# Kernel tuning notes

Measured on AMD Instinct MI355X. Metric: run time of the kernel, lower is better.

The kernel has to match this reference:

```python
import jax, jax.numpy as jnp
import numpy as np

B, LQ, LKV = 2, 2048, 2048
DQ, DKV, HID, NH = 1024, 1024, 1024, 16
HD = HID // NH
EPS = 1e-5


def setup_inputs() -> dict:
    key = jax.random.key(0)
    ks = jax.random.split(key, 12)
    s_q = 1.0 / np.sqrt(DQ)
    s_kv = 1.0 / np.sqrt(DKV)
    s_h = 1.0 / np.sqrt(HID)
    return {
        "query": jax.random.normal(ks[0], (B, LQ, DQ), jnp.float32),
        "key_value": jax.random.normal(ks[1], (B, LKV, DKV), jnp.float32),
        "Wq": jax.random.uniform(ks[2], (DQ, HID), jnp.float32, -s_q, s_q),
        "bq": jax.random.uniform(ks[3], (HID,), jnp.float32, -s_q, s_q),
        "Wk": jax.random.uniform(ks[4], (DKV, HID), jnp.float32, -s_kv, s_kv),
        "bk": jax.random.uniform(ks[5], (HID,), jnp.float32, -s_kv, s_kv),
        "Wv": jax.random.uniform(ks[6], (DKV, HID), jnp.float32, -s_kv, s_kv),
        "bv": jax.random.uniform(ks[7], (HID,), jnp.float32, -s_kv, s_kv),
        "Wo": jax.random.uniform(ks[8], (HID, DQ), jnp.float32, -s_h, s_h),
        "bo": jax.random.uniform(ks[9], (DQ,), jnp.float32, -s_h, s_h),
        "ln_gamma": jnp.ones((DQ,), jnp.float32),
        "ln_beta": jnp.zeros((DQ,), jnp.float32),
    }


def reference(query, key_value, Wq, bq, Wk, bk, Wv, bv, Wo, bo, ln_gamma, ln_beta):
    b, lq, _ = query.shape
    lkv = key_value.shape[1]
    # projections -> [b, heads, len, head_dim]
    Q = (query @ Wq + bq).reshape(b, lq, NH, HD).transpose(0, 2, 1, 3)
    K = (key_value @ Wk + bk).reshape(b, lkv, NH, HD).transpose(0, 2, 1, 3)
    V = (key_value @ Wv + bv).reshape(b, lkv, NH, HD).transpose(0, 2, 1, 3)
    scores = jnp.einsum("bhqd,bhkd->bhqk", Q, K) / jnp.sqrt(jnp.float32(HD))
    attn = jax.nn.softmax(scores, axis=-1)
    ctx = jnp.einsum("bhqk,bhkd->bhqd", attn, V)
    ctx = ctx.transpose(0, 2, 1, 3).reshape(b, lq, HID)
    out = ctx @ Wo + bo
    x = query + out
    mu = jnp.mean(x, axis=-1, keepdims=True)
    var = jnp.mean(jnp.square(x - mu), axis=-1, keepdims=True)
    return (x - mu) / jnp.sqrt(var + EPS) * ln_gamma + ln_beta
```

## Files before the change

kernel.cpp:

```cpp
#include <hip/hip_runtime.h>

typedef unsigned short u16;
typedef __bf16 bf16x8 __attribute__((ext_vector_type(8)));
typedef float f32x4 __attribute__((ext_vector_type(4)));
typedef unsigned short u16x4 __attribute__((ext_vector_type(4)));

#define LOG2E 1.44269504088896340736f
#define LDK 1040
#define LDV 2080
#define EXPM16 12599160.0f

__device__ __forceinline__ u16 f2bf(float f) {
  unsigned u = __float_as_uint(f);
  u += 0x7FFFu + ((u >> 16) & 1u);
  return (u16)(u >> 16);
}

__device__ __forceinline__ void load_lds16(const void* g, void* l) {
  __builtin_amdgcn_global_load_lds(
      (__attribute__((address_space(1))) void*)g,
      (__attribute__((address_space(3))) void*)l, 16, 0, 0);
}

__device__ __forceinline__ f32x4 mfma16(bf16x8 a, bf16x8 b, f32x4 c) {
  return __builtin_amdgcn_mfma_f32_16x16x32_bf16(a, b, c, 0, 0, 0);
}

__global__ __launch_bounds__(256) void pre_kernel(
    const float* __restrict__ q, const float* __restrict__ kv,
    u16* __restrict__ Xq, u16* __restrict__ Xkv,
    const float* __restrict__ Wq, const float* __restrict__ Wk,
    const float* __restrict__ Wv, const float* __restrict__ Wo,
    u16* __restrict__ Wqt, u16* __restrict__ Wkt,
    u16* __restrict__ Wvt, u16* __restrict__ Wot) {
  __shared__ float tile[32][33];
  const int bid = blockIdx.x;
  if (bid < 8192) {
    const int n4each = 4096 * 256;
    int i = bid * 256 + threadIdx.x;
    const float* src; u16* dst; int j;
    if (i < n4each) { src = q; dst = Xq; j = i; }
    else            { src = kv; dst = Xkv; j = i - n4each; }
    const float4 v = ((const float4*)src)[j];
    u16x4 o;
    o.x = f2bf(v.x); o.y = f2bf(v.y); o.z = f2bf(v.z); o.w = f2bf(v.w);
    ((u16x4*)dst)[j] = o;
    return;
  }
  const int t = bid - 8192;
  const int z = t >> 10, rem = t & 1023;
  const float* W; u16* Wt;
  switch (z) {
    case 0: W = Wq; Wt = Wqt; break;
    case 1: W = Wk; Wt = Wkt; break;
    case 2: W = Wv; Wt = Wvt; break;
    default: W = Wo; Wt = Wot; break;
  }
  const int tx = threadIdx.x & 31, ty = threadIdx.x >> 5;
  const int n0 = (rem & 31) * 32, k0 = (rem >> 5) * 32;
#pragma unroll
  for (int i = 0; i < 4; i++)
    tile[ty + i * 8][tx] = W[(size_t)(k0 + ty + i * 8) * 1024 + n0 + tx];
  __syncthreads();
#pragma unroll
  for (int i = 0; i < 4; i++)
    Wt[(size_t)(n0 + ty + i * 8) * 1024 + k0 + tx] = f2bf(tile[tx][ty + i * 8]);
}

__device__ __forceinline__ void gemm_tile(
    const u16* __restrict__ A, int lda, const u16* __restrict__ Bt, int ldb,
    const float* __restrict__ bias, bool brow, float scale,
    u16* __restrict__ Cb, float* __restrict__ Cf,
    int ldc, int bm, int bn, int K) {
  __shared__ alignas(16) u16 As[128 * 32];
  __shared__ alignas(16) u16 Bs[128 * 32];
  const int tid = threadIdx.x;
  const int wave = tid >> 6, lane = tid & 63;
  const int lm = lane & 15, kq = lane >> 4;
  const int g1 = tid, g2 = tid + 256;
  const u16* Ag1 = A + (size_t)(bm + (g1 >> 2)) * lda + (g1 & 3) * 8;
  const u16* Ag2 = A + (size_t)(bm + (g2 >> 2)) * lda + (g2 & 3) * 8;
  const u16* Bg1 = Bt + (size_t)(bn + (g1 >> 2)) * ldb + (g1 & 3) * 8;
  const u16* Bg2 = Bt + (size_t)(bn + (g2 >> 2)) * ldb + (g2 & 3) * 8;
  u16* lA1 = &As[g1 * 8]; u16* lA2 = &As[g2 * 8];
  u16* lB1 = &Bs[g1 * 8]; u16* lB2 = &Bs[g2 * 8];
  const int wm = (wave >> 1) * 64, wn = (wave & 1) * 64;

  f32x4 acc[4][4] = {};
  for (int k0 = 0; k0 < K; k0 += 32) {
    __syncthreads();
    load_lds16(Ag1 + k0, lA1);
    load_lds16(Ag2 + k0, lA2);
    load_lds16(Bg1 + k0, lB1);
    load_lds16(Bg2 + k0, lB2);
    __syncthreads();
    bf16x8 a[4], b[4];
#pragma unroll
    for (int t = 0; t < 4; t++)
      a[t] = *(const bf16x8*)&As[(wm + t * 16 + lm) * 32 + kq * 8];
#pragma unroll
    for (int t = 0; t < 4; t++)
      b[t] = *(const bf16x8*)&Bs[(wn + t * 16 + lm) * 32 + kq * 8];
#pragma unroll
    for (int mt = 0; mt < 4; mt++)
#pragma unroll
      for (int nt = 0; nt < 4; nt++)
        acc[mt][nt] = mfma16(a[mt], b[nt], acc[mt][nt]);
  }
#pragma unroll
  for (int mt = 0; mt < 4; mt++) {
    float rb[4];
#pragma unroll
    for (int r = 0; r < 4; r++)
      rb[r] = (bias && brow) ? bias[bm + wm + mt * 16 + kq * 4 + r] : 0.f;
#pragma unroll
    for (int nt = 0; nt < 4; nt++) {
      const int col = bn + wn + nt * 16 + lm;
      const float cb = (bias && !brow) ? bias[col] : 0.f;
#pragma unroll
      for (int r = 0; r < 4; r++) {
        const int row = bm + wm + mt * 16 + kq * 4 + r;
        const size_t idx = (size_t)row * ldc + col;
        const float v = (acc[mt][nt][r] + rb[r] + cb) * scale;
        if (Cf) Cf[idx] = v;
        else    Cb[idx] = f2bf(v);
      }
    }
  }
}

__global__ __launch_bounds__(256) void proj_gemm_kernel(
    const u16* __restrict__ Xq, const u16* __restrict__ Xkv,
    const u16* __restrict__ Wqt, const u16* __restrict__ Wkt, const u16* __restrict__ Wvt,
    const float* __restrict__ bq, const float* __restrict__ bk, const float* __restrict__ bv,
    u16* __restrict__ Qp, u16* __restrict__ Kp, u16* __restrict__ Vt, float qscale) {
  const int bid = blockIdx.x;
  const u16 *A, *Bt; const float* bias; u16* C;
  bool brow = false; float sc = 1.f; int ldc = 1024; int bm, bn;
  if (bid < 512) {
    const int r = bid & 255;
    const int xcd = r & 7, s = r >> 3;
    bm = (xcd * 4 + (s >> 3)) * 128;
    bn = (s & 7) * 128;
    if (bid < 256) { A = Xq;  Bt = Wqt; bias = bq; C = Qp; sc = qscale; }
    else           { A = Xkv; Bt = Wkt; bias = bk; C = Kp; ldc = LDK;  }
  } else {
    int r = bid - 512;
    const int z = r >> 7; r &= 127;
    const int xcd = r & 7, s = r >> 3;
    bm = (s >> 1) * 128;
    bn = (xcd * 2 + (s & 1)) * 128;
    A = Wvt; Bt = Xkv + (size_t)z * 2048 * 1024; bias = bv; brow = true;
    C = Vt + (size_t)z * 1024 * LDV; ldc = LDV;
  }
  gemm_tile(A, 1024, Bt, 1024, bias, brow, sc, C, nullptr, ldc, bm, bn, 1024);
}

__global__ __launch_bounds__(256) void ogemm_kernel(
    const u16* __restrict__ Ctx, const u16* __restrict__ Wot,
    float* __restrict__ X0, float* __restrict__ X1) {
  const int z = blockIdx.z;
  float* Cf = z ? X1 : X0;
  const int lin = blockIdx.x + 8 * blockIdx.y;
  const int xcd = lin & 7, s = lin >> 3;
  const int bm = (xcd * 4 + (s >> 3)) * 128, bn = (s & 7) * 128;
  gemm_tile(Ctx + z * 512, 1024, Wot + z * 512, 1024, nullptr, false, 1.f,
            nullptr, Cf, 1024, bm, bn, 512);
}

__global__ __launch_bounds__(256) void attn_kernel(
    const u16* __restrict__ Qp, const u16* __restrict__ Kp,
    const u16* __restrict__ Vt, u16* __restrict__ ctx) {
  __shared__ alignas(16) u16 Ks[2 * 64 * 32];
  __shared__ alignas(16) u16 Vs[2 * 64 * 32];
  __shared__ alignas(16) u16 Ps[4][32 * 64];
  const int tid = threadIdx.x;
  const int wave = tid >> 6, lane = tid & 63;
  const int lm = lane & 15, kq = lane >> 4;
  const int L = blockIdx.x;
  const int xcd = L & 7, s = L >> 3;
  const int combo = xcd + 8 * (s >> 4);
  const int qb = s & 15;
  const int h = combo & 15, b = combo >> 4;
  const int qbase = qb * 128 + wave * 32;

  bf16x8 qf[2][2];
#pragma unroll
  for (int qt = 0; qt < 2; qt++)
#pragma unroll
    for (int kc = 0; kc < 2; kc++)
      qf[qt][kc] = *(const bf16x8*)(Qp + (size_t)(b * 2048 + qbase + qt * 16 + lm) * 1024 +
                                    h * 64 + kc * 32 + kq * 8);

  union { u16 u[8]; bf16x8 v; } uo;
#pragma unroll
  for (int i = 0; i < 8; i++) uo.u[i] = 0x3F80;
  const bf16x8 ones = uo.v;

  const u16* Kb = Kp + (size_t)(b * 2048) * LDK + h * 64;
  const u16* Vb = Vt + (size_t)(b * 1024 + h * 64) * LDV;
  u16* Pw = Ps[wave];
  const int pswz = lm & 7;
  const int sp = lane ^ ((lane >> 3) & 7);
  const int c4 = sp >> 2, c3 = sp & 3;
  const int kvsw = ((lm * 4 + kq) ^ (lm >> 1)) * 8;

  f32x4 o[4][2] = {};
  f32x4 lsum[2] = {};

  for (int kv0 = 0; kv0 < 2048; kv0 += 64) {
    __syncthreads();
#pragma unroll
    for (int j = 0; j < 2; j++) {
      const int ii = wave * 2 + j;
      const u16* gk = Kb + (size_t)(kv0 + 16 * (ii & 3) + c4) * LDK + (ii >> 2) * 32 + c3 * 8;
      load_lds16(gk, &Ks[ii * 512 + lane * 8]);
      const u16* gv = Vb + (size_t)(16 * (ii & 3) + c4) * LDV + kv0 + (ii >> 2) * 32 + c3 * 8;
      load_lds16(gv, &Vs[ii * 512 + lane * 8]);
    }
    __syncthreads();

#pragma unroll
    for (int qt = 0; qt < 2; qt++) {
      f32x4 st[4] = {};
#pragma unroll
      for (int kc = 0; kc < 2; kc++)
#pragma unroll
        for (int kvt = 0; kvt < 4; kvt++) {
          const bf16x8 kf = *(const bf16x8*)&Ks[kc * 2048 + kvt * 512 + kvsw];
          st[kvt] = mfma16(kf, qf[qt][kc], st[kvt]);
        }
#pragma unroll
      for (int kvt = 0; kvt < 4; kvt++) {
        const unsigned b0 = __float_as_uint(fmaf(st[kvt][0], 128.f, EXPM16));
        const unsigned b1 = __float_as_uint(fmaf(st[kvt][1], 128.f, EXPM16));
        const unsigned b2 = __float_as_uint(fmaf(st[kvt][2], 128.f, EXPM16));
        const unsigned b3 = __float_as_uint(fmaf(st[kvt][3], 128.f, EXPM16));
        uint2 w;
        w.x = __builtin_amdgcn_perm(b1, b0, 0x05040100u);
        w.y = __builtin_amdgcn_perm(b3, b2, 0x05040100u);
        const int g = (kvt * 2 + (kq >> 1)) ^ pswz;
        *(uint2*)&Pw[(qt * 16 + lm) * 64 + g * 8 + (kq & 1) * 4] = w;
      }
    }
#pragma unroll
    for (int s2 = 0; s2 < 2; s2++) {
      bf16x8 vf[4];
#pragma unroll
      for (int hdt = 0; hdt < 4; hdt++)
        vf[hdt] = *(const bf16x8*)&Vs[s2 * 2048 + hdt * 512 + kvsw];
#pragma unroll
      for (int qt = 0; qt < 2; qt++) {
        const bf16x8 pf =
            *(const bf16x8*)&Pw[(qt * 16 + lm) * 64 + (((s2 * 4 + kq) ^ pswz) * 8)];
        lsum[qt] = mfma16(ones, pf, lsum[qt]);
#pragma unroll
        for (int hdt = 0; hdt < 4; hdt++)
          o[hdt][qt] = mfma16(vf[hdt], pf, o[hdt][qt]);
      }
    }
  }
#pragma unroll
  for (int qt = 0; qt < 2; qt++) {
    const float rl = 1.f / lsum[qt][0];
    u16* cb = ctx + (size_t)(b * 2048 + qbase + qt * 16 + lm) * 1024 + h * 64 + kq * 4;
#pragma unroll
    for (int hdt = 0; hdt < 4; hdt++) {
      u16x4 w;
#pragma unroll
      for (int r = 0; r < 4; r++) w[r] = f2bf(o[hdt][qt][r] * rl);
      *(u16x4*)(cb + hdt * 16) = w;
    }
  }
}

__global__ __launch_bounds__(256) void ln_kernel(
    const float* __restrict__ x0, const float* __restrict__ x1,
    const float* __restrict__ q, const float* __restrict__ bo,
    const float* __restrict__ gamma, const float* __restrict__ beta,
    float* __restrict__ out) {
  const int row = blockIdx.x;
  const int t = threadIdx.x;
  const size_t g = (size_t)row * 256 + t;
  const float4 a = ((const float4*)x0)[g];
  const float4 c = ((const float4*)x1)[g];
  const float4 d = ((const float4*)q)[g];
  const float4 bv = ((const float4*)bo)[t];
  float4 v;
  v.x = a.x + c.x + d.x + bv.x;
  v.y = a.y + c.y + d.y + bv.y;
  v.z = a.z + c.z + d.z + bv.z;
  v.w = a.w + c.w + d.w + bv.w;
  float s = v.x + v.y + v.z + v.w;
  float s2 = v.x * v.x + v.y * v.y + v.z * v.z + v.w * v.w;
#pragma unroll
  for (int m = 1; m < 64; m <<= 1) {
    s += __shfl_xor(s, m);
    s2 += __shfl_xor(s2, m);
  }
  __shared__ float red[8];
  const int wave = t >> 6, lane = t & 63;
  if (lane == 0) { red[wave] = s; red[4 + wave] = s2; }
  __syncthreads();
  s = red[0] + red[1] + red[2] + red[3];
  s2 = red[4] + red[5] + red[6] + red[7];
  const float mu = s * (1.f / 1024.f);
  const float var = s2 * (1.f / 1024.f) - mu * mu;
  const float rstd = rsqrtf(var + 1e-5f);
  const float4 gm = ((const float4*)gamma)[t];
  const float4 bt = ((const float4*)beta)[t];
  float4 o;
  o.x = (v.x - mu) * rstd * gm.x + bt.x;
  o.y = (v.y - mu) * rstd * gm.y + bt.y;
  o.z = (v.z - mu) * rstd * gm.z + bt.z;
  o.w = (v.w - mu) * rstd * gm.w + bt.w;
  ((float4*)(out + (size_t)row * 1024))[t] = o;
}

extern "C" void kernel_launch(void* const* d_in, const int* in_sizes, int n_in,
                              void* d_out, int out_size, void* d_ws, size_t ws_size,
                              hipStream_t stream) {
  const float* query     = (const float*)d_in[0];
  const float* key_value = (const float*)d_in[1];
  const float* Wq = (const float*)d_in[2];
  const float* bq = (const float*)d_in[3];
  const float* Wk = (const float*)d_in[4];
  const float* bk = (const float*)d_in[5];
  const float* Wv = (const float*)d_in[6];
  const float* bv = (const float*)d_in[7];
  const float* Wo = (const float*)d_in[8];
  const float* bo = (const float*)d_in[9];
  const float* gamma = (const float*)d_in[10];
  const float* beta  = (const float*)d_in[11];
  float* out = (float*)d_out;

  const size_t MT = (size_t)4096 * 1024;
  const size_t WT = (size_t)1024 * 1024;
  char* ws = (char*)d_ws;
  u16* Xq  = (u16*)ws; ws += MT * 2;
  u16* Xkv = (u16*)ws; ws += MT * 2;
  u16* Wqt = (u16*)ws; ws += WT * 2;
  u16* Wkt = (u16*)ws; ws += WT * 2;
  u16* Wvt = (u16*)ws; ws += WT * 2;
  u16* Wot = (u16*)ws; ws += WT * 2;
  u16* Qp  = (u16*)ws; ws += MT * 2;
  u16* Kp  = (u16*)ws; ws += (size_t)4096 * LDK * 2;
  u16* Vt  = (u16*)ws; ws += (size_t)2048 * LDV * 2;
  float* X0 = (float*)ws; ws += MT * 4;
  float* X1 = (float*)ws; ws += MT * 4;
  u16* Ctx = Xq;

  const float qscale = 0.125f * LOG2E;

  pre_kernel<<<12288, 256, 0, stream>>>(query, key_value, Xq, Xkv,
                                        Wq, Wk, Wv, Wo, Wqt, Wkt, Wvt, Wot);
  proj_gemm_kernel<<<768, 256, 0, stream>>>(Xq, Xkv, Wqt, Wkt, Wvt, bq, bk, bv,
                                            Qp, Kp, Vt, qscale);
  attn_kernel<<<512, 256, 0, stream>>>(Qp, Kp, Vt, Ctx);
  ogemm_kernel<<<dim3(8, 32, 2), 256, 0, stream>>>(Ctx, Wot, X0, X1);
  ln_kernel<<<4096, 256, 0, stream>>>(X0, X1, query, bo, gamma, beta, out);
}
```

Measured before the change: 223.6 us.

## Double-buffer K/V tiles in attention kernel to overlap loads with compute

Doubles the LDS K and V buffers and issues the global-to-LDS loads for the next 64-key tile before computing on the current one, with one barrier per iteration instead of two. It also raises wave priority around the MFMA section with s_setprio. The aim is to hide global load latency behind the QK^T/PV matrix work. In exchange, LDS use grows, which may reduce occupancy. Correctness depends on the global_load_lds completing before the end-of-iteration barrier, and there is no explicit vmcnt wait before the data is read.

```diff
diff --git a/kernel.cpp b/kernel.cpp
--- a/kernel.cpp
+++ b/kernel.cpp
@@ -171,8 +171,8 @@
 __global__ __launch_bounds__(256) void attn_kernel(
     const u16* __restrict__ Qp, const u16* __restrict__ Kp,
     const u16* __restrict__ Vt, u16* __restrict__ ctx) {
-  __shared__ alignas(16) u16 Ks[2 * 64 * 32];
-  __shared__ alignas(16) u16 Vs[2 * 64 * 32];
+  __shared__ alignas(16) u16 Ks[2 * 4096];
+  __shared__ alignas(16) u16 Vs[2 * 4096];
   __shared__ alignas(16) u16 Ps[4][32 * 64];
   const int tid = threadIdx.x;
   const int wave = tid >> 6, lane = tid & 63;
@@ -208,17 +208,32 @@
   f32x4 o[4][2] = {};
   f32x4 lsum[2] = {};
 
-  for (int kv0 = 0; kv0 < 2048; kv0 += 64) {
-    __syncthreads();
-#pragma unroll
-    for (int j = 0; j < 2; j++) {
-      const int ii = wave * 2 + j;
-      const u16* gk = Kb + (size_t)(kv0 + 16 * (ii & 3) + c4) * LDK + (ii >> 2) * 32 + c3 * 8;
-      load_lds16(gk, &Ks[ii * 512 + lane * 8]);
-      const u16* gv = Vb + (size_t)(16 * (ii & 3) + c4) * LDV + kv0 + (ii >> 2) * 32 + c3 * 8;
-      load_lds16(gv, &Vs[ii * 512 + lane * 8]);
-    }
-    __syncthreads();
+#pragma unroll
+  for (int j = 0; j < 2; j++) {
+    const int ii = wave * 2 + j;
+    const u16* gk = Kb + (size_t)(16 * (ii & 3) + c4) * LDK + (ii >> 2) * 32 + c3 * 8;
+    load_lds16(gk, &Ks[ii * 512 + lane * 8]);
+    const u16* gv = Vb + (size_t)(16 * (ii & 3) + c4) * LDV + (ii >> 2) * 32 + c3 * 8;
+    load_lds16(gv, &Vs[ii * 512 + lane * 8]);
+  }
+  __syncthreads();
+
+  int cur = 0;
+  for (int t = 0; t < 32; ++t) {
+    if (t < 31) {
+      const int kvn = (t + 1) * 64;
+      const int nb = (cur ^ 1) * 4096;
+#pragma unroll
+      for (int j = 0; j < 2; j++) {
+        const int ii = wave * 2 + j;
+        const u16* gk = Kb + (size_t)(kvn + 16 * (ii & 3) + c4) * LDK + (ii >> 2) * 32 + c3 * 8;
+        load_lds16(gk, &Ks[nb + ii * 512 + lane * 8]);
+        const u16* gv = Vb + (size_t)(16 * (ii & 3) + c4) * LDV + kvn + (ii >> 2) * 32 + c3 * 8;
+        load_lds16(gv, &Vs[nb + ii * 512 + lane * 8]);
+      }
+    }
+    const int cb = cur * 4096;
+    __builtin_amdgcn_s_setprio(1);
 
 #pragma unroll
     for (int qt = 0; qt < 2; qt++) {
@@ -227,7 +242,7 @@
       for (int kc = 0; kc < 2; kc++)
 #pragma unroll
         for (int kvt = 0; kvt < 4; kvt++) {
-          const bf16x8 kf = *(const bf16x8*)&Ks[kc * 2048 + kvt * 512 + kvsw];
+          const bf16x8 kf = *(const bf16x8*)&Ks[cb + kc * 2048 + kvt * 512 + kvsw];
           st[kvt] = mfma16(kf, qf[qt][kc], st[kvt]);
         }
 #pragma unroll
@@ -248,7 +263,7 @@
       bf16x8 vf[4];
 #pragma unroll
       for (int hdt = 0; hdt < 4; hdt++)
-        vf[hdt] = *(const bf16x8*)&Vs[s2 * 2048 + hdt * 512 + kvsw];
+        vf[hdt] = *(const bf16x8*)&Vs[cb + s2 * 2048 + hdt * 512 + kvsw];
 #pragma unroll
       for (int qt = 0; qt < 2; qt++) {
         const bf16x8 pf =
@@ -259,17 +274,20 @@
           o[hdt][qt] = mfma16(vf[hdt], pf, o[hdt][qt]);
       }
     }
+    __builtin_amdgcn_s_setprio(0);
+    __syncthreads();
+    cur ^= 1;
   }
 #pragma unroll
   for (int qt = 0; qt < 2; qt++) {
     const float rl = 1.f / lsum[qt][0];
-    u16* cb = ctx + (size_t)(b * 2048 + qbase + qt * 16 + lm) * 1024 + h * 64 + kq * 4;
+    u16* cbp = ctx + (size_t)(b * 2048 + qbase + qt * 16 + lm) * 1024 + h * 64 + kq * 4;
 #pragma unroll
     for (int hdt = 0; hdt < 4; hdt++) {
       u16x4 w;
 #pragma unroll
       for (int r = 0; r < 4; r++) w[r] = f2bf(o[hdt][qt][r] * rl);
-      *(u16x4*)(cb + hdt * 16) = w;
+      *(u16x4*)(cbp + hdt * 16) = w;
     }
   }
 }
```

Result: no change. 221.9 us (-0.8%).
